# Performance work log

Measured on AMD Instinct MI355X. Metric: run time of the kernel, lower is better.

## Reference

```python
import jax, jax.numpy as jnp
import numpy as np

B, L, D = 4096, 200, 64
N_ITEMS, N_USERS, N_RATINGS = 100000, 100000, 5


def setup_inputs() -> dict:
    key = jax.random.key(0)
    ks = jax.random.split(key, 10)
    nodes = jax.random.randint(ks[0], (B,), 0, N_USERS)
    history_uv = jax.random.randint(ks[1], (B, L), 0, N_ITEMS)
    history_r = jax.random.randint(ks[2], (B, L), 0, N_RATINGS)
    s = 1.0 / np.sqrt(D)
    v2e = jax.random.normal(ks[3], (N_ITEMS, D), dtype=jnp.float32)
    r2e = jax.random.normal(ks[4], (N_RATINGS, D), dtype=jnp.float32)
    # torch Linear: weight is [out, in]
    w1_W = jax.random.uniform(ks[5], (D, 2 * D), dtype=jnp.float32, minval=-s, maxval=s)
    w1_b = jax.random.uniform(ks[6], (D,), dtype=jnp.float32, minval=-s, maxval=s)
    w2_W = jax.random.uniform(ks[7], (D, D), dtype=jnp.float32, minval=-s, maxval=s)
    w2_b = jax.random.uniform(ks[8], (D,), dtype=jnp.float32, minval=-s, maxval=s)
    return {
        "v2e": v2e, "r2e": r2e,
        "w1_W": w1_W, "w1_b": w1_b, "w2_W": w2_W, "w2_b": w2_b,
        "nodes": nodes, "history_uv": history_uv, "history_r": history_r,
    }


def reference(v2e, r2e, w1_W, w1_b, w2_W, w2_b, nodes, history_uv, history_r):
    # Gather item and rating embeddings for every (node, history slot): [B, L, D]
    e_uv = v2e[history_uv]
    e_r = r2e[history_r]
    # concat -> [B, L, 2D], two-layer MLP with ReLU
    x = jnp.concatenate([e_uv, e_r], axis=-1)
    h = jax.nn.relu(jnp.einsum("bli,oi->blo", x, w1_W) + w1_b)
    o = jax.nn.relu(jnp.einsum("bli,oi->blo", h, w2_W) + w2_b)
    # uv=True branch: plain mean over the history dimension (nodes/u2e unused)
    return jnp.mean(o, axis=1)  # [B, D]
```

## Files before the change

### kernel.cpp

```cpp
#include <hip/hip_runtime.h>

#define NITEMS 100000
#define NRATE  5
#define BB     4096
#define LL     200
#define DD     64
#define NTILES 6250

typedef short short8  __attribute__((ext_vector_type(8)));
typedef float f32x4   __attribute__((ext_vector_type(4)));
typedef float f32x2   __attribute__((ext_vector_type(2)));
typedef int   i32x4   __attribute__((ext_vector_type(4)));

static __device__ __forceinline__ short f2bf(float f) {
  return (short)((__builtin_bit_cast(unsigned, f) + 0x8000u) >> 16);
}
static __device__ __forceinline__ unsigned pk2bf(float a, float b) {
  const unsigned ua = __builtin_bit_cast(unsigned, a) + 0x8000u;
  const unsigned ub = __builtin_bit_cast(unsigned, b) + 0x8000u;
  return __builtin_amdgcn_perm(ub, ua, 0x07060302u);
}
static __device__ __forceinline__ int kperm(int p) {
  return ((p & 3) << 4) | (p >> 2);
}

#if __has_builtin(__builtin_elementwise_max)
static __device__ __forceinline__ f32x2 relu2(f32x2 v) {
  return __builtin_elementwise_max(v, f32x2{0.f, 0.f});
}
static __device__ __forceinline__ f32x4 relu4(f32x4 v) {
  return __builtin_elementwise_max(v, f32x4{0.f, 0.f, 0.f, 0.f});
}
#else
static __device__ __forceinline__ f32x2 relu2(f32x2 v) {
  return f32x2{fmaxf(v.x, 0.f), fmaxf(v.y, 0.f)};
}
static __device__ __forceinline__ f32x4 relu4(f32x4 v) {
  return f32x4{fmaxf(v[0], 0.f), fmaxf(v[1], 0.f), fmaxf(v[2], 0.f), fmaxf(v[3], 0.f)};
}
#endif

__global__ __launch_bounds__(256) void k_pre(
    const float* __restrict__ v2e, const float* __restrict__ r2e,
    const float* __restrict__ w1W, const float* __restrict__ w1b,
    const float* __restrict__ w2W,
    unsigned char* __restrict__ pre8, short* __restrict__ w2p,
    float* __restrict__ r5p)
{
  const int tid = threadIdx.x;
  const int blk = blockIdx.x;

  if (blk == 0) {
    for (int idx = tid; idx < 64 * 64; idx += 256) {
      const int o = idx >> 6, p = idx & 63;
      w2p[idx] = f2bf(w2W[o * 64 + kperm(p)]);
    }
    for (int idx = tid; idx < NRATE * 64; idx += 256) {
      const int r = idx >> 6, p = idx & 63;
      const int o = kperm(p);
      const float4* wr = reinterpret_cast<const float4*>(w1W + o * 128 + 64);
      const float4* rr = reinterpret_cast<const float4*>(r2e + r * 64);
      float s = w1b[o];
#pragma unroll
      for (int q = 0; q < 16; ++q) {
        const float4 a = wr[q], b = rr[q];
        s += a.x * b.x + a.y * b.y + a.z * b.z + a.w * b.w;
      }
      r5p[r * 64 + p] = s;
    }
    return;
  }

  const int wave = tid >> 6, lane = tid & 63;
  const int n = lane & 15, quad = lane >> 4;
  const int tile = (blk - 1) * 4 + wave;
  if (tile >= NTILES) return;

  const int q0 = ((n >> 1) & 3) * 16 + (n >> 3) * 8 + (n & 1) * 4;

  const size_t row = (size_t)(tile * 16 + n);
  const float4* pv = reinterpret_cast<const float4*>(v2e + row * 64 + quad * 8);
  const float4* qv = reinterpret_cast<const float4*>(v2e + row * 64 + 32 + quad * 8);
  const float4 cur0 = pv[0], cur1 = pv[1], cur2 = qv[0], cur3 = qv[1];

  short8 bfr[2][4];
#pragma unroll
  for (int nt = 0; nt < 4; ++nt)
#pragma unroll
    for (int kh = 0; kh < 2; ++kh) {
      const float4* p = reinterpret_cast<const float4*>(
          w1W + (nt * 16 + n) * 128 + kh * 32 + quad * 8);
      const float4 x0 = p[0], x1 = p[1];
      i32x4 pk = {(int)pk2bf(x0.x, x0.y), (int)pk2bf(x0.z, x0.w),
                  (int)pk2bf(x1.x, x1.y), (int)pk2bf(x1.z, x1.w)};
      bfr[kh][nt] = __builtin_bit_cast(short8, pk);
    }

  short8 afr[2];
  {
    i32x4 pk0 = {(int)pk2bf(cur0.x, cur0.y), (int)pk2bf(cur0.z, cur0.w),
                 (int)pk2bf(cur1.x, cur1.y), (int)pk2bf(cur1.z, cur1.w)};
    afr[0] = __builtin_bit_cast(short8, pk0);
    i32x4 pk1 = {(int)pk2bf(cur2.x, cur2.y), (int)pk2bf(cur2.z, cur2.w),
                 (int)pk2bf(cur3.x, cur3.y), (int)pk2bf(cur3.z, cur3.w)};
    afr[1] = __builtin_bit_cast(short8, pk1);
  }

  f32x4 d[4];
#pragma unroll
  for (int nt = 0; nt < 4; ++nt) {
    f32x4 z = {0.f, 0.f, 0.f, 0.f};
    z = __builtin_amdgcn_mfma_f32_16x16x32_bf16(afr[0], bfr[0][nt], z, 0, 0, 0);
    z = __builtin_amdgcn_mfma_f32_16x16x32_bf16(afr[1], bfr[1][nt], z, 0, 0, 0);
    d[nt] = z;
  }

  const int ib = tile * 16;
#pragma unroll
  for (int r = 0; r < 4; ++r) {
    const int item = ib + quad * 4 + r;
    int pkd = 0;
    pkd = __builtin_amdgcn_cvt_pk_fp8_f32(d[0][r], d[1][r], pkd, false);
    pkd = __builtin_amdgcn_cvt_pk_fp8_f32(d[2][r], d[3][r], pkd, true);
    *reinterpret_cast<int*>(pre8 + (size_t)item * 64 + q0) = pkd;
  }
}

template<int T0, int NT>
static __device__ __forceinline__ void mbody(
    const unsigned char* __restrict__ pre8,
    const int* __restrict__ hu, const int* __restrict__ hr,
    const float* __restrict__ r5w,
    const short8 (&bfr)[2][4], const f32x4 (&zb)[4],
    const int n, const int quad, const float tailm,
    f32x4 (&acc4)[4])
{
  int ivv[NT], irr[NT];
#pragma unroll
  for (int k = 0; k < NT; ++k) {
    const int t = T0 + k;
    const int l = (t == 12) ? min(192 + n, LL - 1) : (t * 16 + n);
    ivv[k] = hu[l];
    irr[k] = hr[l];
  }

  i32x4 g[NT];
#pragma unroll
  for (int k = 0; k < NT; ++k)
    g[k] = *reinterpret_cast<const i32x4*>(
        pre8 + (size_t)ivv[k] * 64 + quad * 16);

#pragma unroll
  for (int k = 0; k < NT; ++k) {
    const float* rbase = r5w + irr[k] * 68 + quad * 8;
    short8 afr[2];
    {
      const f32x2* rp = reinterpret_cast<const f32x2*>(rbase);
      f32x2 p0 = relu2(__builtin_amdgcn_cvt_pk_f32_fp8(g[k][0], false) + rp[0]);
      f32x2 p1 = relu2(__builtin_amdgcn_cvt_pk_f32_fp8(g[k][0], true)  + rp[1]);
      f32x2 p2 = relu2(__builtin_amdgcn_cvt_pk_f32_fp8(g[k][1], false) + rp[2]);
      f32x2 p3 = relu2(__builtin_amdgcn_cvt_pk_f32_fp8(g[k][1], true)  + rp[3]);
      i32x4 hpk = {(int)pk2bf(p0.x, p0.y), (int)pk2bf(p1.x, p1.y),
                   (int)pk2bf(p2.x, p2.y), (int)pk2bf(p3.x, p3.y)};
      afr[0] = __builtin_bit_cast(short8, hpk);
    }
    {
      const f32x2* rp = reinterpret_cast<const f32x2*>(rbase + 32);
      f32x2 p0 = relu2(__builtin_amdgcn_cvt_pk_f32_fp8(g[k][2], false) + rp[0]);
      f32x2 p1 = relu2(__builtin_amdgcn_cvt_pk_f32_fp8(g[k][2], true)  + rp[1]);
      f32x2 p2 = relu2(__builtin_amdgcn_cvt_pk_f32_fp8(g[k][3], false) + rp[2]);
      f32x2 p3 = relu2(__builtin_amdgcn_cvt_pk_f32_fp8(g[k][3], true)  + rp[3]);
      i32x4 hpk = {(int)pk2bf(p0.x, p0.y), (int)pk2bf(p1.x, p1.y),
                   (int)pk2bf(p2.x, p2.y), (int)pk2bf(p3.x, p3.y)};
      afr[1] = __builtin_bit_cast(short8, hpk);
    }

    f32x4 d[4];
#pragma unroll
    for (int nt = 0; nt < 4; ++nt) {
      f32x4 z = zb[nt];
      z = __builtin_amdgcn_mfma_f32_16x16x32_bf16(afr[0], bfr[0][nt], z, 0, 0, 0);
      z = __builtin_amdgcn_mfma_f32_16x16x32_bf16(afr[1], bfr[1][nt], z, 0, 0, 0);
      d[nt] = z;
    }

#pragma unroll
    for (int nt = 0; nt < 4; ++nt) {
      f32x4 mx = relu4(d[nt]);
      if (T0 + k == 12) mx = mx * tailm;
      acc4[nt] += mx;
    }
  }
}

__global__ __launch_bounds__(256) void k_main(
    const unsigned char* __restrict__ pre8, const float* __restrict__ r5p,
    const short* __restrict__ w2p, const float* __restrict__ w2b,
    const int* __restrict__ huv, const int* __restrict__ hrr,
    float* __restrict__ out)
{
  __shared__ __align__(16) float s_r5[4][5 * 68];
  __shared__ float red[4][64];

  const int tid  = threadIdx.x;
  const int wave = tid >> 6, lane = tid & 63;
  const int n = lane & 15, quad = lane >> 4;
  const int hlf = wave & 1;
  const int b = blockIdx.x * 2 + (wave >> 1);

#pragma unroll
  for (int i = 0; i < 5; ++i) {
    const int idx = i * 64 + lane;
    s_r5[wave][(idx >> 6) * 68 + (idx & 63)] = r5p[idx];
  }

  const int* hu = huv + b * LL;
  const int* hr = hrr + b * LL;

  short8 bfr[2][4];
#pragma unroll
  for (int nt = 0; nt < 4; ++nt)
#pragma unroll
    for (int kh = 0; kh < 2; ++kh)
      bfr[kh][nt] = *reinterpret_cast<const short8*>(
          w2p + (nt * 16 + n) * 64 + kh * 32 + quad * 8);

  f32x4 zb[4];
#pragma unroll
  for (int nt = 0; nt < 4; ++nt) {
    const float bv = w2b[nt * 16 + n];
    zb[nt] = f32x4{bv, bv, bv, bv};
  }

  const float tailm = (quad < 2) ? 1.0f : 0.0f;
  f32x4 acc4[4] = {{0.f,0.f,0.f,0.f},{0.f,0.f,0.f,0.f},
                   {0.f,0.f,0.f,0.f},{0.f,0.f,0.f,0.f}};

  if (hlf == 0)
    mbody<0, 7>(pre8, hu, hr, &s_r5[wave][0], bfr, zb, n, quad, tailm, acc4);
  else
    mbody<7, 6>(pre8, hu, hr, &s_r5[wave][0], bfr, zb, n, quad, tailm, acc4);

  float acc[4];
#pragma unroll
  for (int nt = 0; nt < 4; ++nt) {
    float v = (acc4[nt][0] + acc4[nt][1]) + (acc4[nt][2] + acc4[nt][3]);
    v += __shfl_xor(v, 16, 64);
    v += __shfl_xor(v, 32, 64);
    acc[nt] = v;
  }

  red[wave][quad * 16 + n] = acc[quad];
  __syncthreads();
  if (wave < 2) {
    const int bb = blockIdx.x * 2 + wave;
    out[bb * 64 + lane] =
        (red[2 * wave][lane] + red[2 * wave + 1][lane]) * (1.0f / (float)LL);
  }
}

__global__ __launch_bounds__(256) void k_fallback(
    const float* __restrict__ v2e, const float* __restrict__ r2e,
    const float* __restrict__ w1W, const float* __restrict__ w1b,
    const float* __restrict__ w2W, const float* __restrict__ w2b,
    const int* __restrict__ huv, const int* __restrict__ hrr,
    float* __restrict__ out)
{
  __shared__ float sw1[64][129];
  __shared__ float sw2[64][65];
  __shared__ float sx[4][128];
  __shared__ float sh[4][64];
  __shared__ float red[4][64];

  const int tid = threadIdx.x;
  const int wave = tid >> 6, lane = tid & 63;
  const int b = blockIdx.x;

  for (int idx = tid; idx < 64 * 128; idx += 256) sw1[idx >> 7][idx & 127] = w1W[idx];
  for (int idx = tid; idx < 64 * 64; idx += 256) sw2[idx >> 6][idx & 63] = w2W[idx];
  __syncthreads();

  const float b1o = w1b[lane], b2o = w2b[lane];
  float acc = 0.f;

  for (int l = wave; l < LL; l += 4) {
    const int iv = huv[b * LL + l];
    const int ir = hrr[b * LL + l];
    sx[wave][lane]      = v2e[iv * 64 + lane];
    sx[wave][64 + lane] = r2e[ir * 64 + lane];
    __syncthreads();
    float h = b1o;
    for (int i = 0; i < 128; ++i) h += sx[wave][i] * sw1[lane][i];
    sh[wave][lane] = fmaxf(h, 0.f);
    __syncthreads();
    float o = b2o;
    for (int i = 0; i < 64; ++i) o += sh[wave][i] * sw2[lane][i];
    acc += fmaxf(o, 0.f);
  }

  red[wave][lane] = acc;
  __syncthreads();
  if (tid < 64) {
    const float s = red[0][tid] + red[1][tid] + red[2][tid] + red[3][tid];
    out[b * 64 + tid] = s * (1.0f / (float)LL);
  }
}

extern "C" void kernel_launch(void* const* d_in, const int* in_sizes, int n_in,
                              void* d_out, int out_size, void* d_ws, size_t ws_size,
                              hipStream_t stream) {
  (void)in_sizes; (void)n_in; (void)out_size;
  const float* v2e = (const float*)d_in[0];
  const float* r2e = (const float*)d_in[1];
  const float* w1W = (const float*)d_in[2];
  const float* w1b = (const float*)d_in[3];
  const float* w2W = (const float*)d_in[4];
  const float* w2b = (const float*)d_in[5];
  const int* huv = (const int*)d_in[7];
  const int* hrr = (const int*)d_in[8];
  float* out = (float*)d_out;

  const size_t OFF_R5 = (size_t)NITEMS * 64;
  const size_t OFF_W2 = OFF_R5 + NRATE * 64 * sizeof(float);
  const size_t NEED   = OFF_W2 + 64 * 64 * sizeof(short);

  if (ws_size >= NEED) {
    unsigned char* pre8 = (unsigned char*)d_ws;
    float* r5p = (float*)((char*)d_ws + OFF_R5);
    short* w2p = (short*)((char*)d_ws + OFF_W2);

    k_pre<<<1564, 256, 0, stream>>>(v2e, r2e, w1W, w1b, w2W, pre8, w2p, r5p);
    k_main<<<BB / 2, 256, 0, stream>>>(pre8, r5p, w2p, w2b, huv, hrr, out);
  } else {
    k_fallback<<<BB, 256, 0, stream>>>(v2e, r2e, w1W, w1b, w2W, w2b, huv, hrr, out);
  }
}
```

Before: 119.6 us.

## Assign one batch row per wave and hoist all gathers ahead of compute

```diff
diff --git a/kernel.cpp b/kernel.cpp
--- a/kernel.cpp
+++ b/kernel.cpp
@@ -126,73 +126,6 @@
   }
 }
 
-template<int T0, int NT>
-static __device__ __forceinline__ void mbody(
-    const unsigned char* __restrict__ pre8,
-    const int* __restrict__ hu, const int* __restrict__ hr,
-    const float* __restrict__ r5w,
-    const short8 (&bfr)[2][4], const f32x4 (&zb)[4],
-    const int n, const int quad, const float tailm,
-    f32x4 (&acc4)[4])
-{
-  int ivv[NT], irr[NT];
-#pragma unroll
-  for (int k = 0; k < NT; ++k) {
-    const int t = T0 + k;
-    const int l = (t == 12) ? min(192 + n, LL - 1) : (t * 16 + n);
-    ivv[k] = hu[l];
-    irr[k] = hr[l];
-  }
-
-  i32x4 g[NT];
-#pragma unroll
-  for (int k = 0; k < NT; ++k)
-    g[k] = *reinterpret_cast<const i32x4*>(
-        pre8 + (size_t)ivv[k] * 64 + quad * 16);
-
-#pragma unroll
-  for (int k = 0; k < NT; ++k) {
-    const float* rbase = r5w + irr[k] * 68 + quad * 8;
-    short8 afr[2];
-    {
-      const f32x2* rp = reinterpret_cast<const f32x2*>(rbase);
-      f32x2 p0 = relu2(__builtin_amdgcn_cvt_pk_f32_fp8(g[k][0], false) + rp[0]);
-      f32x2 p1 = relu2(__builtin_amdgcn_cvt_pk_f32_fp8(g[k][0], true)  + rp[1]);
-      f32x2 p2 = relu2(__builtin_amdgcn_cvt_pk_f32_fp8(g[k][1], false) + rp[2]);
-      f32x2 p3 = relu2(__builtin_amdgcn_cvt_pk_f32_fp8(g[k][1], true)  + rp[3]);
-      i32x4 hpk = {(int)pk2bf(p0.x, p0.y), (int)pk2bf(p1.x, p1.y),
-                   (int)pk2bf(p2.x, p2.y), (int)pk2bf(p3.x, p3.y)};
-      afr[0] = __builtin_bit_cast(short8, hpk);
-    }
-    {
-      const f32x2* rp = reinterpret_cast<const f32x2*>(rbase + 32);
-      f32x2 p0 = relu2(__builtin_amdgcn_cvt_pk_f32_fp8(g[k][2], false) + rp[0]);
-      f32x2 p1 = relu2(__builtin_amdgcn_cvt_pk_f32_fp8(g[k][2], true)  + rp[1]);
-      f32x2 p2 = relu2(__builtin_amdgcn_cvt_pk_f32_fp8(g[k][3], false) + rp[2]);
-      f32x2 p3 = relu2(__builtin_amdgcn_cvt_pk_f32_fp8(g[k][3], true)  + rp[3]);
-      i32x4 hpk = {(int)pk2bf(p0.x, p0.y), (int)pk2bf(p1.x, p1.y),
-                   (int)pk2bf(p2.x, p2.y), (int)pk2bf(p3.x, p3.y)};
-      afr[1] = __builtin_bit_cast(short8, hpk);
-    }
-
-    f32x4 d[4];
-#pragma unroll
-    for (int nt = 0; nt < 4; ++nt) {
-      f32x4 z = zb[nt];
-      z = __builtin_amdgcn_mfma_f32_16x16x32_bf16(afr[0], bfr[0][nt], z, 0, 0, 0);
-      z = __builtin_amdgcn_mfma_f32_16x16x32_bf16(afr[1], bfr[1][nt], z, 0, 0, 0);
-      d[nt] = z;
-    }
-
-#pragma unroll
-    for (int nt = 0; nt < 4; ++nt) {
-      f32x4 mx = relu4(d[nt]);
-      if (T0 + k == 12) mx = mx * tailm;
-      acc4[nt] += mx;
-    }
-  }
-}
-
 __global__ __launch_bounds__(256) void k_main(
     const unsigned char* __restrict__ pre8, const float* __restrict__ r5p,
     const short* __restrict__ w2p, const float* __restrict__ w2b,
@@ -200,13 +133,32 @@
     float* __restrict__ out)
 {
   __shared__ __align__(16) float s_r5[4][5 * 68];
-  __shared__ float red[4][64];
 
   const int tid  = threadIdx.x;
   const int wave = tid >> 6, lane = tid & 63;
   const int n = lane & 15, quad = lane >> 4;
-  const int hlf = wave & 1;
-  const int b = blockIdx.x * 2 + (wave >> 1);
+  const int b = blockIdx.x * 4 + wave;
+
+  const int* hu = huv + b * LL;
+  const int* hr = hrr + b * LL;
+
+  int iv[13], ir[13];
+#pragma unroll
+  for (int t = 0; t < 12; ++t) {
+    iv[t] = hu[t * 16 + n];
+    ir[t] = hr[t * 16 + n];
+  }
+  {
+    const int lc = min(192 + n, LL - 1);
+    iv[12] = hu[lc];
+    ir[12] = hr[lc];
+  }
+
+  i32x4 g[13];
+#pragma unroll
+  for (int t = 0; t < 13; ++t)
+    g[t] = *reinterpret_cast<const i32x4*>(
+        pre8 + (size_t)iv[t] * 64 + quad * 16);
 
 #pragma unroll
   for (int i = 0; i < 5; ++i) {
@@ -214,9 +166,6 @@
     s_r5[wave][(idx >> 6) * 68 + (idx & 63)] = r5p[idx];
   }
 
-  const int* hu = huv + b * LL;
-  const int* hr = hrr + b * LL;
-
   short8 bfr[2][4];
 #pragma unroll
   for (int nt = 0; nt < 4; ++nt)
@@ -236,10 +185,47 @@
   f32x4 acc4[4] = {{0.f,0.f,0.f,0.f},{0.f,0.f,0.f,0.f},
                    {0.f,0.f,0.f,0.f},{0.f,0.f,0.f,0.f}};
 
-  if (hlf == 0)
-    mbody<0, 7>(pre8, hu, hr, &s_r5[wave][0], bfr, zb, n, quad, tailm, acc4);
-  else
-    mbody<7, 6>(pre8, hu, hr, &s_r5[wave][0], bfr, zb, n, quad, tailm, acc4);
+#pragma unroll
+  for (int t = 0; t < 13; ++t) {
+    const float* rbase = &s_r5[wave][ir[t] * 68 + quad * 8];
+    short8 afr[2];
+    {
+      const f32x2* rp = reinterpret_cast<const f32x2*>(rbase);
+      f32x2 p0 = relu2(__builtin_amdgcn_cvt_pk_f32_fp8(g[t][0], false) + rp[0]);
+      f32x2 p1 = relu2(__builtin_amdgcn_cvt_pk_f32_fp8(g[t][0], true)  + rp[1]);
+      f32x2 p2 = relu2(__builtin_amdgcn_cvt_pk_f32_fp8(g[t][1], false) + rp[2]);
+      f32x2 p3 = relu2(__builtin_amdgcn_cvt_pk_f32_fp8(g[t][1], true)  + rp[3]);
+      i32x4 hpk = {(int)pk2bf(p0.x, p0.y), (int)pk2bf(p1.x, p1.y),
+                   (int)pk2bf(p2.x, p2.y), (int)pk2bf(p3.x, p3.y)};
+      afr[0] = __builtin_bit_cast(short8, hpk);
+    }
+    {
+      const f32x2* rp = reinterpret_cast<const f32x2*>(rbase + 32);
+      f32x2 p0 = relu2(__builtin_amdgcn_cvt_pk_f32_fp8(g[t][2], false) + rp[0]);
+      f32x2 p1 = relu2(__builtin_amdgcn_cvt_pk_f32_fp8(g[t][2], true)  + rp[1]);
+      f32x2 p2 = relu2(__builtin_amdgcn_cvt_pk_f32_fp8(g[t][3], false) + rp[2]);
+      f32x2 p3 = relu2(__builtin_amdgcn_cvt_pk_f32_fp8(g[t][3], true)  + rp[3]);
+      i32x4 hpk = {(int)pk2bf(p0.x, p0.y), (int)pk2bf(p1.x, p1.y),
+                   (int)pk2bf(p2.x, p2.y), (int)pk2bf(p3.x, p3.y)};
+      afr[1] = __builtin_bit_cast(short8, hpk);
+    }
+
+    f32x4 d[4];
+#pragma unroll
+    for (int nt = 0; nt < 4; ++nt) {
+      f32x4 z = zb[nt];
+      z = __builtin_amdgcn_mfma_f32_16x16x32_bf16(afr[0], bfr[0][nt], z, 0, 0, 0);
+      z = __builtin_amdgcn_mfma_f32_16x16x32_bf16(afr[1], bfr[1][nt], z, 0, 0, 0);
+      d[nt] = z;
+    }
+
+#pragma unroll
+    for (int nt = 0; nt < 4; ++nt) {
+      f32x4 mx = relu4(d[nt]);
+      if (t == 12) mx = mx * tailm;
+      acc4[nt] += mx;
+    }
+  }
 
   float acc[4];
 #pragma unroll
@@ -250,13 +236,7 @@
     acc[nt] = v;
   }
 
-  red[wave][quad * 16 + n] = acc[quad];
-  __syncthreads();
-  if (wave < 2) {
-    const int bb = blockIdx.x * 2 + wave;
-    out[bb * 64 + lane] =
-        (red[2 * wave][lane] + red[2 * wave + 1][lane]) * (1.0f / (float)LL);
-  }
+  out[b * 64 + quad * 16 + n] = acc[quad] * (1.0f / (float)LL);
 }
 
 __global__ __launch_bounds__(256) void k_fallback(
@@ -330,7 +310,7 @@
     short* w2p = (short*)((char*)d_ws + OFF_W2);
 
     k_pre<<<1564, 256, 0, stream>>>(v2e, r2e, w1W, w1b, w2W, pre8, w2p, r5p);
-    k_main<<<BB / 2, 256, 0, stream>>>(pre8, r5p, w2p, w2b, huv, hrr, out);
+    k_main<<<BB / 4, 256, 0, stream>>>(pre8, r5p, w2p, w2b, huv, hrr, out);
   } else {
     k_fallback<<<BB, 256, 0, stream>>>(v2e, r2e, w1W, w1b, w2W, w2b, huv, hrr, out);
   }
```

After: 117.0 us. 2.3% less time.
